# Kernel optimization log

Measured on AMD Instinct MI355X. Metric: run time of the kernel, lower is better.

Reference implementation:

```python
import jax, jax.numpy as jnp
import numpy as np

HIDDEN = 4096
INTER = 11008
BATCH, SEQ = 2, 2048


def setup_inputs() -> dict:
    key = jax.random.key(0)
    ks = jax.random.split(key, 7)
    s_h = 1.0 / np.sqrt(HIDDEN)   # nn.Linear default init bound fan_in=HIDDEN
    s_i = 1.0 / np.sqrt(INTER)    # fan_in=INTER for down_proj
    return {
        "hidden_states": jax.random.normal(ks[0], (BATCH, SEQ, HIDDEN), dtype=jnp.float32),
        "w_gate": jax.random.uniform(ks[1], (INTER, HIDDEN), jnp.float32, -s_h, s_h),
        "b_gate": jax.random.uniform(ks[2], (INTER,), jnp.float32, -s_h, s_h),
        "w_up": jax.random.uniform(ks[3], (INTER, HIDDEN), jnp.float32, -s_h, s_h),
        "b_up": jax.random.uniform(ks[4], (INTER,), jnp.float32, -s_h, s_h),
        "w_down": jax.random.uniform(ks[5], (HIDDEN, INTER), jnp.float32, -s_i, s_i),
        "b_down": jax.random.uniform(ks[6], (HIDDEN,), jnp.float32, -s_i, s_i),
    }


def reference(hidden_states, w_gate, b_gate, w_up, b_up, w_down, b_down):
    # SwiGLU MLP: down( silu(gate(x)) * up(x) )
    gate = jax.nn.silu(jnp.einsum("bsh,ih->bsi", hidden_states, w_gate) + b_gate)
    up = jnp.einsum("bsh,ih->bsi", hidden_states, w_up) + b_up
    return jnp.einsum("bsi,hi->bsh", gate * up, w_down) + b_down
```

## Files before the change

### kernel.cpp

```cpp
#include <hip/hip_runtime.h>
#include <hip/hip_bf16.h>


#define M_TOK 4096
#define HID   4096
#define INT_  11008

typedef __attribute__((ext_vector_type(8))) short bf16x8;
typedef __attribute__((ext_vector_type(4))) float f32x4;

__device__ __forceinline__ unsigned short f2bf(float f) {
    union { float f; unsigned int u; } a; a.f = f;
    unsigned int u = a.u;
    u += 0x7fff + ((u >> 16) & 1);
    return (unsigned short)(u >> 16);
}

__device__ __forceinline__ float bf2f(unsigned short h) {
    union { unsigned int u; float f; } a; a.u = ((unsigned int)h) << 16;
    return a.f;
}

__global__ void cvt_f32_bf16(const float* __restrict__ in, unsigned short* __restrict__ out, int n4) {
    int stride = gridDim.x * blockDim.x;
    for (int i = blockIdx.x * blockDim.x + threadIdx.x; i < n4; i += stride) {
        float4 v = ((const float4*)in)[i];
        ushort4 o;
        o.x = f2bf(v.x); o.y = f2bf(v.y); o.z = f2bf(v.z); o.w = f2bf(v.w);
        ((ushort4*)out)[i] = o;
    }
}

#define GLL(gsrc, ldst) \
    __builtin_amdgcn_global_load_lds( \
        (__attribute__((address_space(1))) void*)(gsrc), \
        (__attribute__((address_space(3))) void*)(ldst), 16, 0, 0)

template<int EPI>
__global__ __launch_bounds__(512, 2)
void gemm256(const unsigned short* __restrict__ A,
             const unsigned short* __restrict__ B,
             const float* __restrict__ bias,
             const unsigned short* __restrict__ gbuf,
             void* __restrict__ Cv,
             int M, int N, int K) {
    __shared__ unsigned short lds[2 * 32768];

    const int tid  = threadIdx.x;
    const int lane = tid & 63;
    const int w    = tid >> 6;
    const int wm   = w >> 2;
    const int wn   = w & 3;

    const int ntn = N >> 8;
    const int chunk = gridDim.x >> 3;
    const int sw = (blockIdx.x & 7) * chunk + (blockIdx.x >> 3);
    const int bm = sw / ntn, bn = sw % ntn;

    const unsigned short* Ag = A + (size_t)(bm * 256) * K;
    const unsigned short* Bg = B + (size_t)(bn * 256) * K;

    int offA[2][2], offB[2][2];
#pragma unroll
    for (int h = 0; h < 2; ++h)
#pragma unroll
        for (int i = 0; i < 2; ++i) {
            int sig = i * 512 + tid;
            int r   = sig >> 3;
            int s   = (sig & 7) ^ (r & 7);
            int grow = ((r >> 6) * 2 + h) * 64 + (r & 63);
            int gcol = ((r >> 5) * 2 + h) * 32 + (r & 31);
            offA[h][i] = grow * K + s * 8;
            offB[h][i] = gcol * K + s * 8;
        }

    const int rl = lane & 15;
    const int kg = lane >> 4;
    const int x  = rl & 7;
    const int aRow = (wm * 64 + rl) * 64;
    const int bRow = 16384 + (wn * 32 + rl) * 64;
    int slt[2];
#pragma unroll
    for (int ks = 0; ks < 2; ++ks) slt[ks] = ((ks * 4 + kg) ^ x) * 8;

    f32x4 acc[2][2][8];
#pragma unroll
    for (int qm = 0; qm < 2; ++qm)
#pragma unroll
        for (int qn = 0; qn < 2; ++qn)
#pragma unroll
            for (int f = 0; f < 8; ++f)
                acc[qm][qn][f] = (f32x4){0.f, 0.f, 0.f, 0.f};

    const int NT = K >> 6;

#define STAGE_A(H, DST, SRC) \
    GLL((SRC) + offA[H][0], (DST) + (H) * 8192 + tid * 8); \
    GLL((SRC) + offA[H][1], (DST) + (H) * 8192 + 4096 + tid * 8)
#define STAGE_B(H, DST, SRC) \
    GLL((SRC) + offB[H][0], (DST) + 16384 + (H) * 8192 + tid * 8); \
    GLL((SRC) + offB[H][1], (DST) + 16384 + (H) * 8192 + 4096 + tid * 8)

    {
        unsigned short* d0 = lds;
        STAGE_A(0, d0, Ag); STAGE_B(0, d0, Bg); STAGE_B(1, d0, Bg); STAGE_A(1, d0, Ag);
    }
    asm volatile("s_waitcnt vmcnt(0)" ::: "memory");
    __builtin_amdgcn_s_barrier();

#define RD_A(QM) \
    { _Pragma("unroll") for (int ks = 0; ks < 2; ++ks) \
      _Pragma("unroll") for (int fm = 0; fm < 4; ++fm) \
        aK[ks * 4 + fm] = *(const bf16x8*)(bc + (QM) * 8192 + aRow + fm * 1024 + slt[ks]); }
#define RD_B(QN, BB) \
    { _Pragma("unroll") for (int ks = 0; ks < 2; ++ks) \
      _Pragma("unroll") for (int fn = 0; fn < 2; ++fn) \
        BB[ks * 2 + fn] = *(const bf16x8*)(bc + (QN) * 8192 + bRow + fn * 1024 + slt[ks]); }
#define Q16(QM, QN, BB) \
    { __builtin_amdgcn_s_setprio(1); \
      _Pragma("unroll") for (int ks = 0; ks < 2; ++ks) \
      _Pragma("unroll") for (int fm = 0; fm < 4; ++fm) \
      _Pragma("unroll") for (int fn = 0; fn < 2; ++fn) \
        acc[QM][QN][fm * 2 + fn] = __builtin_amdgcn_mfma_f32_16x16x32_bf16( \
            aK[ks * 4 + fm], BB[ks * 2 + fn], acc[QM][QN][fm * 2 + fn], 0, 0, 0); \
      __builtin_amdgcn_s_setprio(0); }
#define LGKM0 \
    asm volatile("s_waitcnt lgkmcnt(0)" ::: "memory"); \
    __builtin_amdgcn_sched_barrier(0)

    for (int t = 0; t < NT; ++t) {
        const unsigned short* bc = lds + (t & 1) * 32768;
        unsigned short* sb = lds + ((t + 1) & 1) * 32768;
        const int ts = (t + 1 < NT) ? (t + 1) : (NT - 1);
        const unsigned short* sAt = Ag + (size_t)ts * 64;
        const unsigned short* sBt = Bg + (size_t)ts * 64;

        bf16x8 aK[8], b0[4], b1[4];

        RD_A(0); RD_B(0, b0);
        STAGE_A(0, sb, sAt);
        __builtin_amdgcn_s_barrier();
        LGKM0;
        Q16(0, 0, b0);
        asm volatile("s_waitcnt vmcnt(2)" ::: "memory");
        __builtin_amdgcn_s_barrier();

        RD_B(1, b1);
        STAGE_B(0, sb, sBt);
        __builtin_amdgcn_s_barrier();
        LGKM0;
        Q16(0, 1, b1);
        __builtin_amdgcn_s_barrier();

        RD_A(1);
        STAGE_B(1, sb, sBt);
        __builtin_amdgcn_s_barrier();
        LGKM0;
        Q16(1, 1, b1);
        __builtin_amdgcn_s_barrier();

        STAGE_A(1, sb, sAt);
        __builtin_amdgcn_s_barrier();
        Q16(1, 0, b0);
        asm volatile("s_waitcnt vmcnt(4)" ::: "memory");
        __builtin_amdgcn_s_barrier();
    }
#undef RD_A
#undef RD_B
#undef Q16
#undef LGKM0
#undef STAGE_A
#undef STAGE_B

    const int rbase = bm * 256 + wm * 128 + (lane >> 4) * 4;
    const int cbase = bn * 256 + wn * 64 + (lane & 15);
#pragma unroll
    for (int qm = 0; qm < 2; ++qm)
#pragma unroll
        for (int qn = 0; qn < 2; ++qn)
#pragma unroll
            for (int fn = 0; fn < 2; ++fn) {
                const int col = cbase + qn * 32 + fn * 16;
                const float bv = bias[col];
#pragma unroll
                for (int fm = 0; fm < 4; ++fm) {
                    const int rb = rbase + qm * 64 + fm * 16;
#pragma unroll
                    for (int j = 0; j < 4; ++j) {
                        const size_t idx = (size_t)(rb + j) * (size_t)N + col;
                        float v = acc[qm][qn][fm * 2 + fn][j] + bv;
                        if (EPI == 0) {
                            ((unsigned short*)Cv)[idx] = f2bf(v);
                        } else if (EPI == 1) {
                            float g = bf2f(gbuf[idx]);
                            float s = g / (1.f + __expf(-g));
                            ((unsigned short*)Cv)[idx] = f2bf(s * v);
                        } else {
                            ((float*)Cv)[idx] = v;
                        }
                    }
                }
            }
}

extern "C" void kernel_launch(void* const* d_in, const int* in_sizes, int n_in,
                              void* d_out, int out_size, void* d_ws, size_t ws_size,
                              hipStream_t stream) {
    const float* x  = (const float*)d_in[0];
    const float* wg = (const float*)d_in[1];
    const float* bg = (const float*)d_in[2];
    const float* wu = (const float*)d_in[3];
    const float* bu = (const float*)d_in[4];
    const float* wd = (const float*)d_in[5];
    const float* bd = (const float*)d_in[6];

    const size_t NX = (size_t)M_TOK * HID;
    const size_t NW = (size_t)INT_ * HID;

    unsigned short* ws = (unsigned short*)d_ws;
    unsigned short* Xb = ws;
    unsigned short* S1 = Xb + NX;
    unsigned short* S2 = S1 + NW;
    unsigned short* S3 = S2 + NW;

    dim3 blk512(512);
    dim3 blk256(256);
    const int CG = 2048;

    cvt_f32_bf16<<<CG, blk256, 0, stream>>>(x,  Xb, (int)(NX / 4));
    cvt_f32_bf16<<<CG, blk256, 0, stream>>>(wg, S1, (int)(NW / 4));
    gemm256<0><<<dim3(16 * 43), blk512, 0, stream>>>(Xb, S1, bg, (const unsigned short*)nullptr,
                                                     (void*)S2, M_TOK, INT_, HID);
    cvt_f32_bf16<<<CG, blk256, 0, stream>>>(wu, S3, (int)(NW / 4));
    gemm256<1><<<dim3(16 * 43), blk512, 0, stream>>>(Xb, S3, bu, S2,
                                                     (void*)S1, M_TOK, INT_, HID);
    cvt_f32_bf16<<<CG, blk256, 0, stream>>>(wd, S2, (int)(NW / 4));
    gemm256<2><<<dim3(16 * 16), blk512, 0, stream>>>(S1, S2, bd, (const unsigned short*)nullptr,
                                                     d_out, M_TOK, HID, INT_);
}
```

Baseline: 1.137 ms.

## Double-buffer MFMA register fragments and prefetch next tile's A fragment

Splits the per-iteration A/B fragment registers into separate A0/A1/B0/B1 sets. The next K-tile's first A fragment is loaded from LDS at the end of the current iteration. The explicit lgkmcnt(0) waits are removed and the vmcnt waits are moved so that LDS reads overlap with MFMA work and global-to-LDS staging. This is meant to hide LDS read latency behind matrix math. In exchange it raises register pressure under launch_bounds(512,2), which could cause spills or lower occupancy.

```diff
diff --git a/kernel.cpp b/kernel.cpp
--- a/kernel.cpp
+++ b/kernel.cpp
@@ -101,32 +101,32 @@
     GLL((SRC) + offB[H][0], (DST) + 16384 + (H) * 8192 + tid * 8); \
     GLL((SRC) + offB[H][1], (DST) + 16384 + (H) * 8192 + 4096 + tid * 8)
 
-    {
-        unsigned short* d0 = lds;
-        STAGE_A(0, d0, Ag); STAGE_B(0, d0, Bg); STAGE_B(1, d0, Bg); STAGE_A(1, d0, Ag);
-    }
-    asm volatile("s_waitcnt vmcnt(0)" ::: "memory");
-    __builtin_amdgcn_s_barrier();
-
-#define RD_A(QM) \
+#define RD_A(BUF, QM, DST) \
     { _Pragma("unroll") for (int ks = 0; ks < 2; ++ks) \
       _Pragma("unroll") for (int fm = 0; fm < 4; ++fm) \
-        aK[ks * 4 + fm] = *(const bf16x8*)(bc + (QM) * 8192 + aRow + fm * 1024 + slt[ks]); }
-#define RD_B(QN, BB) \
+        DST[ks * 4 + fm] = *(const bf16x8*)((BUF) + (QM) * 8192 + aRow + fm * 1024 + slt[ks]); }
+#define RD_B(BUF, QN, DST) \
     { _Pragma("unroll") for (int ks = 0; ks < 2; ++ks) \
       _Pragma("unroll") for (int fn = 0; fn < 2; ++fn) \
-        BB[ks * 2 + fn] = *(const bf16x8*)(bc + (QN) * 8192 + bRow + fn * 1024 + slt[ks]); }
-#define Q16(QM, QN, BB) \
+        DST[ks * 2 + fn] = *(const bf16x8*)((BUF) + (QN) * 8192 + bRow + fn * 1024 + slt[ks]); }
+#define Q16(QM, QN, AF, BF) \
     { __builtin_amdgcn_s_setprio(1); \
       _Pragma("unroll") for (int ks = 0; ks < 2; ++ks) \
       _Pragma("unroll") for (int fm = 0; fm < 4; ++fm) \
       _Pragma("unroll") for (int fn = 0; fn < 2; ++fn) \
         acc[QM][QN][fm * 2 + fn] = __builtin_amdgcn_mfma_f32_16x16x32_bf16( \
-            aK[ks * 4 + fm], BB[ks * 2 + fn], acc[QM][QN][fm * 2 + fn], 0, 0, 0); \
+            AF[ks * 4 + fm], BF[ks * 2 + fn], acc[QM][QN][fm * 2 + fn], 0, 0, 0); \
       __builtin_amdgcn_s_setprio(0); }
-#define LGKM0 \
-    asm volatile("s_waitcnt lgkmcnt(0)" ::: "memory"); \
-    __builtin_amdgcn_sched_barrier(0)
+#define VMC2 asm volatile("s_waitcnt vmcnt(2)" ::: "memory")
+#define BARR __builtin_amdgcn_s_barrier()
+#define PIN  __builtin_amdgcn_sched_barrier(0)
+
+    bf16x8 A0f[4 * 2], A1f[4 * 2], B0f[2 * 2], B1f[2 * 2];
+
+    STAGE_A(0, lds, Ag); STAGE_B(0, lds, Bg); STAGE_B(1, lds, Bg); STAGE_A(1, lds, Ag);
+    VMC2;
+    BARR; PIN;
+    RD_A(lds, 0, A0f);
 
     for (int t = 0; t < NT; ++t) {
         const unsigned short* bc = lds + (t & 1) * 32768;
@@ -135,40 +135,39 @@
         const unsigned short* sAt = Ag + (size_t)ts * 64;
         const unsigned short* sBt = Bg + (size_t)ts * 64;
 
-        bf16x8 aK[8], b0[4], b1[4];
-
-        RD_A(0); RD_B(0, b0);
+        RD_B(bc, 0, B0f);
+        RD_B(bc, 1, B1f);
         STAGE_A(0, sb, sAt);
-        __builtin_amdgcn_s_barrier();
-        LGKM0;
-        Q16(0, 0, b0);
-        asm volatile("s_waitcnt vmcnt(2)" ::: "memory");
-        __builtin_amdgcn_s_barrier();
-
-        RD_B(1, b1);
+        BARR;
+        Q16(0, 0, A0f, B0f);
+        VMC2;
+        BARR; PIN;
+
+        RD_A(bc, 1, A1f);
         STAGE_B(0, sb, sBt);
-        __builtin_amdgcn_s_barrier();
-        LGKM0;
-        Q16(0, 1, b1);
-        __builtin_amdgcn_s_barrier();
-
-        RD_A(1);
+        BARR;
+        Q16(0, 1, A0f, B1f);
+        BARR; PIN;
+
         STAGE_B(1, sb, sBt);
-        __builtin_amdgcn_s_barrier();
-        LGKM0;
-        Q16(1, 1, b1);
-        __builtin_amdgcn_s_barrier();
-
+        BARR;
+        Q16(1, 1, A1f, B1f);
+        VMC2;
+        BARR; PIN;
+
+        RD_A(sb, 0, A0f);
         STAGE_A(1, sb, sAt);
-        __builtin_amdgcn_s_barrier();
-        Q16(1, 0, b0);
-        asm volatile("s_waitcnt vmcnt(4)" ::: "memory");
-        __builtin_amdgcn_s_barrier();
+        BARR;
+        Q16(1, 0, A1f, B0f);
+        VMC2;
+        BARR; PIN;
     }
 #undef RD_A
 #undef RD_B
 #undef Q16
-#undef LGKM0
+#undef VMC2
+#undef BARR
+#undef PIN
 #undef STAGE_A
 #undef STAGE_B
 
```

Measured after the change: 1.139 ms. Within noise of the previous version (+0.2%).
